# Performance work log

Measured on AMD Instinct MI355X. Metric: run time of the kernel, lower is better.

Reference implementation:

```python
import jax, jax.numpy as jnp
import numpy as np

D = 64
G = 200
U = 4000
P = 4000
B = 512
LAYERS = 1


def setup_inputs() -> dict:
    key = jax.random.key(0)
    ks = jax.random.split(key, 8)
    xav = 1.0 / np.sqrt(D)
    return {
        "train_interaction": jax.random.uniform(ks[0], (U + P, U + P), dtype=jnp.float32),
        "g_u_interaction": jax.random.uniform(ks[1], (G + U, G + U), dtype=jnp.float32),
        "g_p_interaction": jax.random.uniform(ks[2], (G + P, G + P), dtype=jnp.float32),
        "user_emb": jax.random.normal(ks[3], (U, D), dtype=jnp.float32) * xav,
        "paper_emb": jax.random.normal(ks[4], (P, D), dtype=jnp.float32) * xav,
        "group_emb": jax.random.normal(ks[5], (G, D), dtype=jnp.float32) * xav,
        "W_attn": jax.random.normal(ks[6], (D, D), dtype=jnp.float32) * xav,
        "user_ids": jax.random.randint(ks[7], (B,), 0, U, dtype=jnp.int32),
    }


def _propagate(adj, x, layers):
    # LightGCN-style: row-normalized propagation, mean over layer outputs (incl. layer 0)
    deg = jnp.sum(adj, axis=1, keepdims=True)
    adj_n = adj / jnp.maximum(deg, 1e-8)
    acc = x
    h = x
    for _ in range(layers):
        h = adj_n @ h
        acc = acc + h
    return acc / (layers + 1)


def reference(train_interaction, g_u_interaction, g_p_interaction, user_emb, paper_emb, group_emb, W_attn, user_ids):
    u_p = _propagate(train_interaction, jnp.concatenate([user_emb, paper_emb], 0), LAYERS)
    g_u = _propagate(g_u_interaction, jnp.concatenate([group_emb, user_emb], 0), LAYERS)
    g_p = _propagate(g_p_interaction, jnp.concatenate([group_emb, paper_emb], 0), LAYERS)
    n_user, n_group = user_emb.shape[0], group_emb.shape[0]
    u_p_u, u_p_p = u_p[:n_user], u_p[n_user:]          # [U,D], [P,D]
    g_u_u = g_u[n_group:]                               # [U,D]
    g_p_p = g_p[n_group:]                               # [P,D]
    user_feat = ((u_p_u + g_u_u) * 0.5)[user_ids]       # [B,D]
    # per-paper two-view features, batched over all papers at once
    i_feat = jnp.stack([u_p_p, g_p_p], axis=1)          # [P,2,D]
    scale = 1.0 / jnp.sqrt(jnp.asarray(user_feat.shape[-1], user_feat.dtype))
    q = user_feat @ W_attn                               # [B,D]
    logits = jnp.einsum('bd,pkd->bpk', q, i_feat) * scale  # [B,P,2]
    attn = jax.nn.softmax(logits, axis=-1)
    dots = jnp.einsum('bd,pkd->bpk', user_feat, i_feat)    # [B,P,2]
    scores = jnp.sum(attn * dots, axis=-1)                  # [B,P]
    return scores, user_feat
```

## Files before the change

kernel.cpp:

```cpp
#include <hip/hip_runtime.h>

typedef float f32x4 __attribute__((ext_vector_type(4)));
typedef __bf16 bf16x8 __attribute__((ext_vector_type(8)));
typedef unsigned short u16;


constexpr size_t OFF_XTT = 0;
constexpr size_t OFF_XGU = OFF_XTT + (size_t)64 * 8000 * 2;
constexpr size_t OFF_XGP = OFF_XGU + (size_t)64 * 4224 * 2;
constexpr size_t OFF_P0  = OFF_XGP + (size_t)64 * 4224 * 2;
constexpr size_t OFF_P1  = OFF_P0 + (size_t)4 * 512 * 64 * 4;
constexpr size_t OFF_P2  = OFF_P1 + (size_t)4 * 4000 * 64 * 4;
constexpr size_t OFF_P3  = OFF_P2 + (size_t)3 * 512 * 64 * 4;
constexpr size_t OFF_D0  = OFF_P3 + (size_t)3 * 4000 * 64 * 4;
constexpr size_t OFF_D1  = OFF_D0 + (size_t)4 * 512 * 4;
constexpr size_t OFF_D2  = OFF_D1 + (size_t)4 * 4000 * 4;
constexpr size_t OFF_D3  = OFF_D2 + (size_t)3 * 512 * 4;
constexpr size_t OFF_UPU = OFF_D3 + (size_t)3 * 4000 * 4;
constexpr size_t OFF_GUU = OFF_UPU + (size_t)512 * 64 * 4;
constexpr size_t OFF_UPB = OFF_GUU + (size_t)512 * 64 * 4;
constexpr size_t OFF_GPB = OFF_UPB + (size_t)4000 * 64 * 2;
constexpr size_t OFF_UFB = OFF_GPB + (size_t)4000 * 64 * 2;
constexpr size_t OFF_QB  = OFF_UFB + (size_t)512 * 64 * 2;

static __device__ __forceinline__ u16 f2bf(float f) {
    union { float f; unsigned u; } v; v.f = f;
    unsigned r = v.u + 0x7FFFu + ((v.u >> 16) & 1u);
    return (u16)(r >> 16);
}

__global__ __launch_bounds__(256) void build_xT(const float* __restrict__ ue,
                                                const float* __restrict__ pe,
                                                const float* __restrict__ ge,
                                                char* __restrict__ ws) {
    __shared__ float tile[64 * 65];
    int wg = blockIdx.x, tid = threadIdx.x;
    int t, kt;
    if (wg < 125)      { t = 0; kt = wg; }
    else if (wg < 191) { t = 1; kt = wg - 125; }
    else               { t = 2; kt = wg - 191; }
    int k0 = kt * 64;
#pragma unroll
    for (int rep = 0; rep < 16; ++rep) {
        int e = rep * 256 + tid;
        int r = e >> 6, c = e & 63;
        int k = k0 + r;
        float v;
        if (t == 0)      v = (k < 4000) ? ue[(size_t)k * 64 + c] : pe[(size_t)(k - 4000) * 64 + c];
        else if (t == 1) v = (k < 200) ? ge[(size_t)k * 64 + c] : ((k < 4200) ? ue[(size_t)(k - 200) * 64 + c] : 0.0f);
        else             v = (k < 200) ? ge[(size_t)k * 64 + c] : ((k < 4200) ? pe[(size_t)(k - 200) * 64 + c] : 0.0f);
        tile[r * 65 + c] = v;
    }
    __syncthreads();
    u16* dst; int Kpad;
    if (t == 0)      { dst = (u16*)(ws + OFF_XTT); Kpad = 8000; }
    else if (t == 1) { dst = (u16*)(ws + OFF_XGU); Kpad = 4224; }
    else             { dst = (u16*)(ws + OFF_XGP); Kpad = 4224; }
#pragma unroll
    for (int rep = 0; rep < 16; ++rep) {
        int e = rep * 256 + tid;
        int n = e >> 6, kk = e & 63;
        dst[(size_t)n * Kpad + k0 + kk] = f2bf(tile[kk * 65 + n]);
    }
}

__global__ __launch_bounds__(256) void prop_kernel(const float* __restrict__ adjT,
                                                   const float* __restrict__ adjGU,
                                                   const float* __restrict__ adjGP,
                                                   const int* __restrict__ uids,
                                                   char* __restrict__ ws) {
    int wid = blockIdx.x * 4 + (threadIdx.x >> 6);
    if (wid >= 1974) return;
    int lane = threadIdx.x & 63;
    int m = lane & 15, quad = lane >> 4;

    int job, rowtile, chunk;
    if (wid < 128)       { job = 0; rowtile = wid >> 2; chunk = wid & 3; }
    else if (wid < 1128) { int t = wid - 128;  job = 1; rowtile = t >> 2; chunk = t & 3; }
    else if (wid < 1224) { int t = wid - 1128; job = 2; rowtile = t / 3; chunk = t - rowtile * 3; }
    else                 { int t = wid - 1224; job = 3; rowtile = t / 3; chunk = t - rowtile * 3; }

    const float* adj; const u16* xT; float* part; float* degp;
    int adjK, Kpad, sb, se, rowg;
    int row_local = rowtile * 16 + m;
    if (job <= 1) {
        adj = adjT; adjK = 8000; Kpad = 8000; xT = (const u16*)(ws + OFF_XTT);
        sb = chunk * 63; se = (sb + 63 < 250) ? sb + 63 : 250;
        if (job == 0) {
            rowg = uids[row_local];
            part = (float*)(ws + OFF_P0) + ((size_t)chunk * 512 + rowtile * 16) * 64;
            degp = (float*)(ws + OFF_D0) + chunk * 512 + rowtile * 16;
        } else {
            rowg = 4000 + row_local;
            part = (float*)(ws + OFF_P1) + ((size_t)chunk * 4000 + rowtile * 16) * 64;
            degp = (float*)(ws + OFF_D1) + chunk * 4000 + rowtile * 16;
        }
    } else {
        adjK = 4200; Kpad = 4224;
        sb = chunk * 44; se = sb + 44;
        if (job == 2) {
            adj = adjGU; xT = (const u16*)(ws + OFF_XGU);
            rowg = 200 + uids[row_local];
            part = (float*)(ws + OFF_P2) + ((size_t)chunk * 512 + rowtile * 16) * 64;
            degp = (float*)(ws + OFF_D2) + chunk * 512 + rowtile * 16;
        } else {
            adj = adjGP; xT = (const u16*)(ws + OFF_XGP);
            rowg = 200 + row_local;
            part = (float*)(ws + OFF_P3) + ((size_t)chunk * 4000 + rowtile * 16) * 64;
            degp = (float*)(ws + OFF_D3) + chunk * 4000 + rowtile * 16;
        }
    }

    const float* arow = adj + (size_t)rowg * adjK;
    const u16* xb0 = xT + (size_t)m * Kpad + quad * 8;
    const size_t bstride = (size_t)16 * Kpad;

    f32x4 acc[4];
#pragma unroll
    for (int nt = 0; nt < 4; ++nt) acc[nt] = (f32x4){0.f, 0.f, 0.f, 0.f};
    float degsum = 0.f;

#pragma unroll 2
    for (int s = sb; s < se; ++s) {
        int k0 = s * 32 + quad * 8;
        float a[8];
        if (k0 + 8 <= adjK) {
            f32x4 v0 = __builtin_nontemporal_load((const f32x4*)(arow + k0));
            f32x4 v1 = __builtin_nontemporal_load((const f32x4*)(arow + k0 + 4));
            a[0] = v0[0]; a[1] = v0[1]; a[2] = v0[2]; a[3] = v0[3];
            a[4] = v1[0]; a[5] = v1[1]; a[6] = v1[2]; a[7] = v1[3];
        } else {
#pragma unroll
            for (int j = 0; j < 8; ++j) a[j] = (k0 + j < adjK) ? arow[k0 + j] : 0.0f;
        }
        degsum += ((a[0] + a[1]) + (a[2] + a[3])) + ((a[4] + a[5]) + (a[6] + a[7]));
        union { u16 h[8]; bf16x8 v; } af;
#pragma unroll
        for (int j = 0; j < 8; ++j) af.h[j] = f2bf(a[j]);
        const u16* bp = xb0 + s * 32;
#pragma unroll
        for (int nt = 0; nt < 4; ++nt) {
            bf16x8 bf = *(const bf16x8*)(bp + nt * bstride);
            acc[nt] = __builtin_amdgcn_mfma_f32_16x16x32_bf16(af.v, bf, acc[nt], 0, 0, 0);
        }
    }

    degsum += __shfl_xor(degsum, 16, 64);
    degsum += __shfl_xor(degsum, 32, 64);
    if (lane < 16) degp[lane] = degsum;

#pragma unroll
    for (int nt = 0; nt < 4; ++nt)
#pragma unroll
        for (int r = 0; r < 4; ++r)
            part[(size_t)(quad * 4 + r) * 64 + nt * 16 + m] = acc[nt][r];
}

__global__ __launch_bounds__(256) void epi1(const float* __restrict__ ue,
                                            const float* __restrict__ pe,
                                            const int* __restrict__ uids,
                                            char* __restrict__ ws) {
    int e = blockIdx.x * 256 + threadIdx.x;
    if (e >= 9024 * 64) return;
    int row = e >> 6, c = e & 63;
    const float* part; const float* degp; const float* xsrc;
    int nch, r, nrows;
    float* outf = nullptr; u16* outh = nullptr;
    if (row < 512) {
        r = row; nch = 4; nrows = 512;
        part = (const float*)(ws + OFF_P0); degp = (const float*)(ws + OFF_D0);
        xsrc = ue + (size_t)uids[r] * 64;
        outf = (float*)(ws + OFF_UPU) + (size_t)r * 64;
    } else if (row < 4512) {
        r = row - 512; nch = 4; nrows = 4000;
        part = (const float*)(ws + OFF_P1); degp = (const float*)(ws + OFF_D1);
        xsrc = pe + (size_t)r * 64;
        outh = (u16*)(ws + OFF_UPB) + (size_t)r * 64;
    } else if (row < 5024) {
        r = row - 4512; nch = 3; nrows = 512;
        part = (const float*)(ws + OFF_P2); degp = (const float*)(ws + OFF_D2);
        xsrc = ue + (size_t)uids[r] * 64;
        outf = (float*)(ws + OFF_GUU) + (size_t)r * 64;
    } else {
        r = row - 5024; nch = 3; nrows = 4000;
        part = (const float*)(ws + OFF_P3); degp = (const float*)(ws + OFF_D3);
        xsrc = pe + (size_t)r * 64;
        outh = (u16*)(ws + OFF_GPB) + (size_t)r * 64;
    }
    float dot = 0.f, deg = 0.f;
    for (int cc = 0; cc < nch; ++cc) {
        dot += part[((size_t)cc * nrows + r) * 64 + c];
        deg += degp[(size_t)cc * nrows + r];
    }
    float res = 0.5f * (xsrc[c] + dot / fmaxf(deg, 1e-8f));
    if (outf) outf[c] = res; else outh[c] = f2bf(res);
}

__global__ __launch_bounds__(256) void epi2(const float* __restrict__ W,
                                            float* __restrict__ dout,
                                            char* __restrict__ ws) {
    int e = blockIdx.x * 256 + threadIdx.x;
    int b = e >> 6, n = e & 63;
    const float* upu = (const float*)(ws + OFF_UPU);
    const float* guu = (const float*)(ws + OFF_GUU);
    float uf = 0.5f * (upu[(size_t)b * 64 + n] + guu[(size_t)b * 64 + n]);
    dout[(size_t)512 * 4000 + e] = uf;
    ((u16*)(ws + OFF_UFB))[e] = f2bf(uf);
    float q = 0.f;
#pragma unroll 8
    for (int d = 0; d < 64; ++d)
        q += 0.5f * (upu[(size_t)b * 64 + d] + guu[(size_t)b * 64 + d]) * W[d * 64 + n];
    ((u16*)(ws + OFF_QB))[e] = f2bf(q * 0.125f);
}

__global__ __launch_bounds__(256) void attn(char* __restrict__ ws,
                                            float* __restrict__ dout) {
    int wid = blockIdx.x * 4 + (threadIdx.x >> 6);
    if (wid >= 8000) return;
    int lane = threadIdx.x & 63, m = lane & 15, quad = lane >> 4;
    int btile = wid / 250, ptile = wid - btile * 250;

    const u16* qr = (const u16*)(ws + OFF_QB)  + ((size_t)btile * 16 + m) * 64 + quad * 8;
    const u16* ur = (const u16*)(ws + OFF_UFB) + ((size_t)btile * 16 + m) * 64 + quad * 8;
    const u16* pr = (const u16*)(ws + OFF_UPB) + ((size_t)ptile * 16 + m) * 64 + quad * 8;
    const u16* gr = (const u16*)(ws + OFF_GPB) + ((size_t)ptile * 16 + m) * 64 + quad * 8;

    f32x4 s1 = (f32x4){0.f,0.f,0.f,0.f}, s2 = s1, d1 = s1, d2 = s1;
#pragma unroll
    for (int ks = 0; ks < 2; ++ks) {
        bf16x8 qf  = *(const bf16x8*)(qr + ks * 32);
        bf16x8 uff = *(const bf16x8*)(ur + ks * 32);
        bf16x8 upf = *(const bf16x8*)(pr + ks * 32);
        bf16x8 gpf = *(const bf16x8*)(gr + ks * 32);
        s1 = __builtin_amdgcn_mfma_f32_16x16x32_bf16(qf,  upf, s1, 0, 0, 0);
        s2 = __builtin_amdgcn_mfma_f32_16x16x32_bf16(qf,  gpf, s2, 0, 0, 0);
        d1 = __builtin_amdgcn_mfma_f32_16x16x32_bf16(uff, upf, d1, 0, 0, 0);
        d2 = __builtin_amdgcn_mfma_f32_16x16x32_bf16(uff, gpf, d2, 0, 0, 0);
    }
#pragma unroll
    for (int r = 0; r < 4; ++r) {
        int b = btile * 16 + quad * 4 + r;
        int p = ptile * 16 + m;
        float l0 = s1[r], l1 = s2[r];
        float mx = fmaxf(l0, l1);
        float e0 = __expf(l0 - mx), e1 = __expf(l1 - mx);
        dout[(size_t)b * 4000 + p] = (e0 * d1[r] + e1 * d2[r]) / (e0 + e1);
    }
}

extern "C" void kernel_launch(void* const* d_in, const int* in_sizes, int n_in,
                              void* d_out, int out_size, void* d_ws, size_t ws_size,
                              hipStream_t stream) {
    const float* adjT  = (const float*)d_in[0];
    const float* adjGU = (const float*)d_in[1];
    const float* adjGP = (const float*)d_in[2];
    const float* ue    = (const float*)d_in[3];
    const float* pe    = (const float*)d_in[4];
    const float* ge    = (const float*)d_in[5];
    const float* W     = (const float*)d_in[6];
    const int*   uids  = (const int*)d_in[7];
    char* ws = (char*)d_ws;
    float* dout = (float*)d_out;

    hipLaunchKernelGGL(build_xT, dim3(257), dim3(256), 0, stream, ue, pe, ge, ws);
    hipLaunchKernelGGL(prop_kernel, dim3(494), dim3(256), 0, stream, adjT, adjGU, adjGP, uids, ws);
    hipLaunchKernelGGL(epi1, dim3((9024 * 64) / 256), dim3(256), 0, stream, ue, pe, uids, ws);
    hipLaunchKernelGGL(epi2, dim3(128), dim3(256), 0, stream, W, dout, ws);
    hipLaunchKernelGGL(attn, dim3(2000), dim3(256), 0, stream, ws, dout);
}
```

Measured before the change: 474.9 us.

## Double split-K chunks and software-pipeline adjacency loads in propagation kernel

Doubles the split-K factor of the propagation GEMM (8 chunks for the 8000-wide adjacency, 6 for the 4200-wide ones), which doubles the wave count and the partial buffers that epi1 reduces. The inner loop is rewritten to prefetch the next step's adjacency and embedding tiles before computing the current MFMAs, and the ragged tail step is peeled out. The aim is more memory-level parallelism on this bandwidth-bound read of the large dense adjacency matrices. In exchange it uses more registers and adds extra partial-sum traffic and reduction work in the epilogue.

```diff
diff --git a/kernel.cpp b/kernel.cpp
--- a/kernel.cpp
+++ b/kernel.cpp
@@ -9,14 +9,14 @@
 constexpr size_t OFF_XGU = OFF_XTT + (size_t)64 * 8000 * 2;
 constexpr size_t OFF_XGP = OFF_XGU + (size_t)64 * 4224 * 2;
 constexpr size_t OFF_P0  = OFF_XGP + (size_t)64 * 4224 * 2;
-constexpr size_t OFF_P1  = OFF_P0 + (size_t)4 * 512 * 64 * 4;
-constexpr size_t OFF_P2  = OFF_P1 + (size_t)4 * 4000 * 64 * 4;
-constexpr size_t OFF_P3  = OFF_P2 + (size_t)3 * 512 * 64 * 4;
-constexpr size_t OFF_D0  = OFF_P3 + (size_t)3 * 4000 * 64 * 4;
-constexpr size_t OFF_D1  = OFF_D0 + (size_t)4 * 512 * 4;
-constexpr size_t OFF_D2  = OFF_D1 + (size_t)4 * 4000 * 4;
-constexpr size_t OFF_D3  = OFF_D2 + (size_t)3 * 512 * 4;
-constexpr size_t OFF_UPU = OFF_D3 + (size_t)3 * 4000 * 4;
+constexpr size_t OFF_P1  = OFF_P0 + (size_t)8 * 512 * 64 * 4;
+constexpr size_t OFF_P2  = OFF_P1 + (size_t)8 * 4000 * 64 * 4;
+constexpr size_t OFF_P3  = OFF_P2 + (size_t)6 * 512 * 64 * 4;
+constexpr size_t OFF_D0  = OFF_P3 + (size_t)6 * 4000 * 64 * 4;
+constexpr size_t OFF_D1  = OFF_D0 + (size_t)8 * 512 * 4;
+constexpr size_t OFF_D2  = OFF_D1 + (size_t)8 * 4000 * 4;
+constexpr size_t OFF_D3  = OFF_D2 + (size_t)6 * 512 * 4;
+constexpr size_t OFF_UPU = OFF_D3 + (size_t)6 * 4000 * 4;
 constexpr size_t OFF_GUU = OFF_UPU + (size_t)512 * 64 * 4;
 constexpr size_t OFF_UPB = OFF_GUU + (size_t)512 * 64 * 4;
 constexpr size_t OFF_GPB = OFF_UPB + (size_t)4000 * 64 * 2;
@@ -64,28 +64,28 @@
     }
 }
 
-__global__ __launch_bounds__(256) void prop_kernel(const float* __restrict__ adjT,
-                                                   const float* __restrict__ adjGU,
-                                                   const float* __restrict__ adjGP,
-                                                   const int* __restrict__ uids,
-                                                   char* __restrict__ ws) {
+__global__ __launch_bounds__(256, 4) void prop_kernel(const float* __restrict__ adjT,
+                                                      const float* __restrict__ adjGU,
+                                                      const float* __restrict__ adjGP,
+                                                      const int* __restrict__ uids,
+                                                      char* __restrict__ ws) {
     int wid = blockIdx.x * 4 + (threadIdx.x >> 6);
-    if (wid >= 1974) return;
+    if (wid >= 3948) return;
     int lane = threadIdx.x & 63;
     int m = lane & 15, quad = lane >> 4;
 
     int job, rowtile, chunk;
-    if (wid < 128)       { job = 0; rowtile = wid >> 2; chunk = wid & 3; }
-    else if (wid < 1128) { int t = wid - 128;  job = 1; rowtile = t >> 2; chunk = t & 3; }
-    else if (wid < 1224) { int t = wid - 1128; job = 2; rowtile = t / 3; chunk = t - rowtile * 3; }
-    else                 { int t = wid - 1224; job = 3; rowtile = t / 3; chunk = t - rowtile * 3; }
+    if (wid < 256)       { job = 0; rowtile = wid >> 3; chunk = wid & 7; }
+    else if (wid < 2256) { int t = wid - 256;  job = 1; rowtile = t >> 3; chunk = t & 7; }
+    else if (wid < 2448) { int t = wid - 2256; job = 2; rowtile = t / 6; chunk = t - rowtile * 6; }
+    else                 { int t = wid - 2448; job = 3; rowtile = t / 6; chunk = t - rowtile * 6; }
 
     const float* adj; const u16* xT; float* part; float* degp;
     int adjK, Kpad, sb, se, rowg;
     int row_local = rowtile * 16 + m;
     if (job <= 1) {
         adj = adjT; adjK = 8000; Kpad = 8000; xT = (const u16*)(ws + OFF_XTT);
-        sb = chunk * 63; se = (sb + 63 < 250) ? sb + 63 : 250;
+        sb = chunk * 32; se = (sb + 32 < 250) ? sb + 32 : 250;
         if (job == 0) {
             rowg = uids[row_local];
             part = (float*)(ws + OFF_P0) + ((size_t)chunk * 512 + rowtile * 16) * 64;
@@ -97,7 +97,7 @@
         }
     } else {
         adjK = 4200; Kpad = 4224;
-        sb = chunk * 44; se = sb + 44;
+        sb = chunk * 22; se = sb + 22;
         if (job == 2) {
             adj = adjGU; xT = (const u16*)(ws + OFF_XGU);
             rowg = 200 + uids[row_local];
@@ -120,28 +120,66 @@
     for (int nt = 0; nt < 4; ++nt) acc[nt] = (f32x4){0.f, 0.f, 0.f, 0.f};
     float degsum = 0.f;
 
-#pragma unroll 2
-    for (int s = sb; s < se; ++s) {
-        int k0 = s * 32 + quad * 8;
+    bool irreg = (job >= 2) && (se == 132);
+    int se_v = irreg ? 131 : se;
+
+    f32x4 a0, a1; bf16x8 bcur[4];
+    {
+        const float* ap = arow + sb * 32 + quad * 8;
+        a0 = __builtin_nontemporal_load((const f32x4*)ap);
+        a1 = __builtin_nontemporal_load((const f32x4*)(ap + 4));
+        const u16* bp = xb0 + sb * 32;
+#pragma unroll
+        for (int nt = 0; nt < 4; ++nt) bcur[nt] = *(const bf16x8*)(bp + nt * bstride);
+    }
+
+#define PROP_COMPUTE()                                                          \
+    {                                                                           \
+        degsum += ((a0[0] + a0[1]) + (a0[2] + a0[3]))                           \
+                + ((a1[0] + a1[1]) + (a1[2] + a1[3]));                          \
+        union { u16 h[8]; bf16x8 v; } af;                                       \
+        af.h[0] = f2bf(a0[0]); af.h[1] = f2bf(a0[1]);                           \
+        af.h[2] = f2bf(a0[2]); af.h[3] = f2bf(a0[3]);                           \
+        af.h[4] = f2bf(a1[0]); af.h[5] = f2bf(a1[1]);                           \
+        af.h[6] = f2bf(a1[2]); af.h[7] = f2bf(a1[3]);                           \
+        acc[0] = __builtin_amdgcn_mfma_f32_16x16x32_bf16(af.v, bcur[0], acc[0], 0, 0, 0); \
+        acc[1] = __builtin_amdgcn_mfma_f32_16x16x32_bf16(af.v, bcur[1], acc[1], 0, 0, 0); \
+        acc[2] = __builtin_amdgcn_mfma_f32_16x16x32_bf16(af.v, bcur[2], acc[2], 0, 0, 0); \
+        acc[3] = __builtin_amdgcn_mfma_f32_16x16x32_bf16(af.v, bcur[3], acc[3], 0, 0, 0); \
+    }
+
+    for (int s = sb; s < se_v - 1; ++s) {
+        const float* ap = arow + (s + 1) * 32 + quad * 8;
+        f32x4 na0 = __builtin_nontemporal_load((const f32x4*)ap);
+        f32x4 na1 = __builtin_nontemporal_load((const f32x4*)(ap + 4));
+        bf16x8 nb[4];
+        const u16* bp = xb0 + (s + 1) * 32;
+#pragma unroll
+        for (int nt = 0; nt < 4; ++nt) nb[nt] = *(const bf16x8*)(bp + nt * bstride);
+
+        PROP_COMPUTE();
+
+        a0 = na0; a1 = na1;
+#pragma unroll
+        for (int nt = 0; nt < 4; ++nt) bcur[nt] = nb[nt];
+    }
+    PROP_COMPUTE();
+#undef PROP_COMPUTE
+
+    if (irreg) {
+        int k0 = 131 * 32 + quad * 8;
         float a[8];
-        if (k0 + 8 <= adjK) {
-            f32x4 v0 = __builtin_nontemporal_load((const f32x4*)(arow + k0));
-            f32x4 v1 = __builtin_nontemporal_load((const f32x4*)(arow + k0 + 4));
-            a[0] = v0[0]; a[1] = v0[1]; a[2] = v0[2]; a[3] = v0[3];
-            a[4] = v1[0]; a[5] = v1[1]; a[6] = v1[2]; a[7] = v1[3];
-        } else {
-#pragma unroll
-            for (int j = 0; j < 8; ++j) a[j] = (k0 + j < adjK) ? arow[k0 + j] : 0.0f;
-        }
+#pragma unroll
+        for (int j = 0; j < 8; ++j) a[j] = (k0 + j < adjK) ? arow[k0 + j] : 0.0f;
         degsum += ((a[0] + a[1]) + (a[2] + a[3])) + ((a[4] + a[5]) + (a[6] + a[7]));
         union { u16 h[8]; bf16x8 v; } af;
 #pragma unroll
         for (int j = 0; j < 8; ++j) af.h[j] = f2bf(a[j]);
-        const u16* bp = xb0 + s * 32;
+        const u16* bp = xb0 + 131 * 32;
 #pragma unroll
         for (int nt = 0; nt < 4; ++nt) {
-            bf16x8 bf = *(const bf16x8*)(bp + nt * bstride);
-            acc[nt] = __builtin_amdgcn_mfma_f32_16x16x32_bf16(af.v, bf, acc[nt], 0, 0, 0);
+            bf16x8 bv = *(const bf16x8*)(bp + nt * bstride);
+            acc[nt] = __builtin_amdgcn_mfma_f32_16x16x32_bf16(af.v, bv, acc[nt], 0, 0, 0);
         }
     }
 
@@ -167,22 +205,22 @@
     int nch, r, nrows;
     float* outf = nullptr; u16* outh = nullptr;
     if (row < 512) {
-        r = row; nch = 4; nrows = 512;
+        r = row; nch = 8; nrows = 512;
         part = (const float*)(ws + OFF_P0); degp = (const float*)(ws + OFF_D0);
         xsrc = ue + (size_t)uids[r] * 64;
         outf = (float*)(ws + OFF_UPU) + (size_t)r * 64;
     } else if (row < 4512) {
-        r = row - 512; nch = 4; nrows = 4000;
+        r = row - 512; nch = 8; nrows = 4000;
         part = (const float*)(ws + OFF_P1); degp = (const float*)(ws + OFF_D1);
         xsrc = pe + (size_t)r * 64;
         outh = (u16*)(ws + OFF_UPB) + (size_t)r * 64;
     } else if (row < 5024) {
-        r = row - 4512; nch = 3; nrows = 512;
+        r = row - 4512; nch = 6; nrows = 512;
         part = (const float*)(ws + OFF_P2); degp = (const float*)(ws + OFF_D2);
         xsrc = ue + (size_t)uids[r] * 64;
         outf = (float*)(ws + OFF_GUU) + (size_t)r * 64;
     } else {
-        r = row - 5024; nch = 3; nrows = 4000;
+        r = row - 5024; nch = 6; nrows = 4000;
         part = (const float*)(ws + OFF_P3); degp = (const float*)(ws + OFF_D3);
         xsrc = pe + (size_t)r * 64;
         outh = (u16*)(ws + OFF_GPB) + (size_t)r * 64;
@@ -263,7 +301,7 @@
     float* dout = (float*)d_out;
 
     hipLaunchKernelGGL(build_xT, dim3(257), dim3(256), 0, stream, ue, pe, ge, ws);
-    hipLaunchKernelGGL(prop_kernel, dim3(494), dim3(256), 0, stream, adjT, adjGU, adjGP, uids, ws);
+    hipLaunchKernelGGL(prop_kernel, dim3(987), dim3(256), 0, stream, adjT, adjGU, adjGP, uids, ws);
     hipLaunchKernelGGL(epi1, dim3((9024 * 64) / 256), dim3(256), 0, stream, ue, pe, uids, ws);
     hipLaunchKernelGGL(epi2, dim3(128), dim3(256), 0, stream, W, dout, ws);
     hipLaunchKernelGGL(attn, dim3(2000), dim3(256), 0, stream, ws, dout);
```

New measurement: 484.7 us. 2.1% more time.
